# Optimization experiments

Hardware: AMD Instinct MI355X
Metric: run time of the kernel (lower is better)

The kernel has to match this reference:

```python
import jax, jax.numpy as jnp
import numpy as np

NUM_HEADS = 16

def setup_inputs() -> dict:
    key = jax.random.key(0)
    k1, k2, k3 = jax.random.split(key, 3)
    B, N, C = 4, 1024, 1024
    x = jax.random.normal(k1, (B, N, C), dtype=jnp.float32)
    w_qkv = jax.random.normal(k2, (C, 3 * C), dtype=jnp.float32) * (C ** -0.5)
    b_qkv = jnp.zeros((3 * C,), dtype=jnp.float32)
    w_proj = jax.random.normal(k3, (C, C), dtype=jnp.float32) * (C ** -0.5)
    b_proj = jnp.zeros((C,), dtype=jnp.float32)
    return {"x": x, "w_qkv": w_qkv, "b_qkv": b_qkv, "w_proj": w_proj, "b_proj": b_proj}

def reference(x, w_qkv, b_qkv, w_proj, b_proj):
    B, N, C = x.shape
    H = NUM_HEADS
    D = C // H
    scale = D ** -0.5
    # qkv projection: [B,N,3C] -> [3,B,H,N,D]
    qkv = (x @ w_qkv + b_qkv).reshape(B, N, 3, H, D).transpose(2, 0, 3, 1, 4)
    q, k, v = qkv[0], qkv[1], qkv[2]
    q = q * scale
    attn = jnp.einsum('bhnd,bhmd->bhnm', q, k)  # full N x N scores
    attn = jax.nn.softmax(attn, axis=-1)
    out = jnp.einsum('bhnm,bhmd->bhnd', attn, v)  # [B,H,N,D]
    out = out.transpose(0, 2, 1, 3).reshape(B, N, C)
    return out @ w_proj + b_proj
```

## Files before the change

kernel.cpp:

```cpp
#include <hip/hip_runtime.h>

typedef unsigned short u16;
typedef unsigned int u32;
typedef __attribute__((ext_vector_type(8))) short bf16x8;
typedef __attribute__((ext_vector_type(4))) float f32x4;
typedef __attribute__((ext_vector_type(16))) float f32x16;

#define LOG2E 1.4426950408889634f
#define QSCALE (0.125f * LOG2E)

__device__ __forceinline__ u16 f2bf(float f) {
  union { float f; u32 u; } x; x.f = f;
  u32 r = x.u + 0x7fffu + ((x.u >> 16) & 1u);
  return (u16)(r >> 16);
}

__device__ __forceinline__ u32 cvtpk(float a, float b) {
  u32 r;
  asm("v_cvt_pk_bf16_f32 %0, %1, %2" : "=v"(r) : "v"(a), "v"(b));
  return r;
}

__device__ __forceinline__ bf16x8 mkfrag(u32 a, u32 b, u32 c, u32 d) {
  union { u32 w[4]; bf16x8 v; } u;
  u.w[0] = a; u.w[1] = b; u.w[2] = c; u.w[3] = d;
  return u.v;
}

__device__ __forceinline__ void gload_lds16(const void* g, void* l) {
  __builtin_amdgcn_global_load_lds((const __attribute__((address_space(1))) u32*)g,
                                   (__attribute__((address_space(3))) u32*)l, 16, 0, 0);
}

__global__ __launch_bounds__(256) void k_cvt_x(const float* __restrict__ in, u16* __restrict__ out) {
  int i = blockIdx.x * 256 + threadIdx.x;
  const float4* p = (const float4*)in;
  float4 a = p[i * 2], b = p[i * 2 + 1];
  uint4 o;
  o.x = (u32)f2bf(a.x) | ((u32)f2bf(a.y) << 16);
  o.y = (u32)f2bf(a.z) | ((u32)f2bf(a.w) << 16);
  o.z = (u32)f2bf(b.x) | ((u32)f2bf(b.y) << 16);
  o.w = (u32)f2bf(b.z) | ((u32)f2bf(b.w) << 16);
  ((uint4*)out)[i] = o;
}

__global__ __launch_bounds__(256) void k_transpose_cvt(const float* __restrict__ src, u16* __restrict__ dst,
                                                       int R, int Cc) {
  __shared__ float tile[32][33];
  int c0 = blockIdx.x * 32, r0 = blockIdx.y * 32;
  int tx = threadIdx.x, ty = threadIdx.y;
  #pragma unroll
  for (int j = 0; j < 4; ++j)
    tile[ty * 4 + j][tx] = src[(r0 + ty * 4 + j) * Cc + c0 + tx];
  __syncthreads();
  #pragma unroll
  for (int j = 0; j < 4; ++j) {
    int cl = ty * 4 + j;
    dst[(c0 + cl) * R + r0 + tx] = f2bf(tile[tx][cl]);
  }
}

template <int EPI, int NBN>
__global__ __launch_bounds__(512) void k_gemm(const u16* __restrict__ A, const u16* __restrict__ Bt,
                                              const float* __restrict__ bias,
                                              u16* __restrict__ oq, u16* __restrict__ ok,
                                              u16* __restrict__ ovt, float* __restrict__ of) {
  __shared__ u16 lds[24576];
  const int tid = threadIdx.x;
  const int l = tid & 63, w = tid >> 6;
  const int wm = w >> 2, wn = w & 3;
  const int lr = l & 15, lh = l >> 4;
  const int cpx = gridDim.x >> 3;
  const int wg = (blockIdx.x & 7) * cpx + (blockIdx.x >> 3);
  const int bn = wg % NBN, bm = wg / NBN;

  f32x4 acc[4][2] = {};
  const int e = tid * 8;
  const int srow = e >> 5;
  const int sgr  = (e >> 3) & 3;
  const int scol = (sgr ^ ((srow >> 1) & 3)) * 8;
  const u16* gA = A + (bm * 128 + srow) * 1024 + scol;
  const u16* gB = Bt + (bn * 128 + srow) * 1024 + scol;

  #define GSTAGE(kk, b)                                              \
    do {                                                             \
      gload_lds16(gA + (kk), lds + (b) * 8192 + e);                  \
      gload_lds16(gB + (kk), lds + (b) * 8192 + 4096 + e);           \
    } while (0)

  GSTAGE(0, 0);
  GSTAGE(32, 1);
  int cur = 0, nxt = 2;

  for (int it = 0; it < 32; ++it) {
    if (it < 31) asm volatile("s_waitcnt vmcnt(2)" ::: "memory");
    else         asm volatile("s_waitcnt vmcnt(0)" ::: "memory");
    __builtin_amdgcn_s_barrier();
    __builtin_amdgcn_sched_barrier(0);

    if (it < 30) GSTAGE((it + 2) * 32, nxt);

    const u16* Asc = lds + cur * 8192;
    bf16x8 af[4], bfr[2];
    #pragma unroll
    for (int mi = 0; mi < 4; ++mi) {
      int r = wm * 64 + mi * 16 + lr;
      af[mi] = *(const bf16x8*)(Asc + r * 32 + ((lh ^ ((r >> 1) & 3)) * 8));
    }
    #pragma unroll
    for (int ni = 0; ni < 2; ++ni) {
      int r = wn * 32 + ni * 16 + lr;
      bfr[ni] = *(const bf16x8*)(Asc + 4096 + r * 32 + ((lh ^ ((r >> 1) & 3)) * 8));
    }
    #pragma unroll
    for (int mi = 0; mi < 4; ++mi)
      #pragma unroll
      for (int ni = 0; ni < 2; ++ni)
        acc[mi][ni] = __builtin_amdgcn_mfma_f32_16x16x32_bf16(af[mi], bfr[ni], acc[mi][ni], 0, 0, 0);

    cur = (cur == 2) ? 0 : cur + 1;
    nxt = (nxt == 2) ? 0 : nxt + 1;
  }
  #undef GSTAGE

  if (EPI == 0) {
    #pragma unroll
    for (int ni = 0; ni < 2; ++ni) {
      int col = bn * 128 + wn * 32 + ni * 16 + lr;
      float bb = bias[col];
      #pragma unroll
      for (int mi = 0; mi < 4; ++mi) {
        int row = bm * 128 + wm * 64 + mi * 16 + lh * 4;
        #pragma unroll
        for (int r = 0; r < 4; ++r)
          of[(row + r) * (NBN * 128) + col] = acc[mi][ni][r] + bb;
      }
    }
  } else {
    const int s = bn >> 3;
    __syncthreads();
    if (s < 2) {
      u16* dst = (s == 0) ? oq : ok;
      const float sc = (s == 0) ? QSCALE : 1.0f;
      #pragma unroll
      for (int ni = 0; ni < 2; ++ni) {
        int cl = wn * 32 + ni * 16 + lr;
        float bb = bias[bn * 128 + cl];
        #pragma unroll
        for (int mi = 0; mi < 4; ++mi) {
          int rl = wm * 64 + mi * 16 + lh * 4;
          #pragma unroll
          for (int r = 0; r < 4; ++r)
            lds[(rl + r) * 136 + cl] = f2bf((acc[mi][ni][r] + bb) * sc);
        }
      }
      __syncthreads();
      const int row = tid >> 2, q4 = tid & 3;
      const int h0 = ((bn * 128) & 1023) >> 6;
      const int b = (bm * 128) >> 10, n0 = (bm * 128) & 1023;
      const u16* srow2 = lds + row * 136 + q4 * 32;
      u16* drow = dst + ((u32)((b * 16 + h0 + (q4 >> 1)) * 1024) + n0 + row) * 64 + (q4 & 1) * 32;
      #pragma unroll
      for (int j = 0; j < 4; ++j)
        *(uint4*)(drow + j * 8) = *(const uint4*)(srow2 + j * 8);
    } else {
      #pragma unroll
      for (int ni = 0; ni < 2; ++ni) {
        int cl = wn * 32 + ni * 16 + lr;
        float bb = bias[bn * 128 + cl];
        #pragma unroll
        for (int mi = 0; mi < 4; ++mi) {
          int rl = wm * 64 + mi * 16 + lh * 4;
          u32 p0 = (u32)f2bf(acc[mi][ni][0] + bb) | ((u32)f2bf(acc[mi][ni][1] + bb) << 16);
          u32 p1 = (u32)f2bf(acc[mi][ni][2] + bb) | ((u32)f2bf(acc[mi][ni][3] + bb) << 16);
          uint2 pk; pk.x = p0; pk.y = p1;
          *(uint2*)(lds + cl * 136 + rl) = pk;
        }
      }
      __syncthreads();
      const int cl = tid >> 2, q4 = tid & 3;
      const int c = bn * 128 + cl, cc = c & 1023, h = cc >> 6, d = cc & 63;
      const int b = (bm * 128) >> 10, n0 = (bm * 128) & 1023;
      const u16* srow2 = lds + cl * 136 + q4 * 32;
      u16* drow = ovt + ((b * 16 + h) * 64 + d) * 1024 + n0 + q4 * 32;
      #pragma unroll
      for (int j = 0; j < 4; ++j)
        *(uint4*)(drow + j * 8) = *(const uint4*)(srow2 + j * 8);
    }
  }
}

__global__ __launch_bounds__(256) void k_attn(const u16* __restrict__ q, const u16* __restrict__ k,
                                              const u16* __restrict__ vt, u16* __restrict__ ao) {
  __shared__ u16 Ks[2][4096], Vs[2][4096];
  const int tid = threadIdx.x, l = tid & 63, w = tid >> 6;
  const int lq = l & 31;
  const int hi = l >> 5;
  const int i = blockIdx.x;
  const int bh = (i & 7) * 8 + ((i >> 3) & 7);
  const int qb = i >> 6;

  const int qrow = qb * 128 + w * 32 + lq;
  const u16* qg = q + bh * 65536 + qrow * 64;
  bf16x8 qf[4];
  #pragma unroll
  for (int ks = 0; ks < 4; ++ks)
    qf[ks] = *(const bf16x8*)(qg + ks * 16 + hi * 8);

  float mr = -1e30f, lsum = 0.f;
  f32x16 o0 = {}, o1 = {};

  const u16* kg = k + bh * 65536;
  const u16* vg = vt + bh * 65536;

  const int ch0 = tid, ch1 = 256 + tid;
  const int r0_ = ch0 >> 3, s0_ = (ch0 & 7) ^ (r0_ & 7);
  const int r1_ = ch1 >> 3, s1_ = (ch1 & 7) ^ (r1_ & 7);

  #define STAGE(t, buf)                                                        \
    do {                                                                       \
      gload_lds16(kg + (t) * 4096 + r0_ * 64 + s0_ * 8, Ks[buf] + ch0 * 8);    \
      gload_lds16(vg + r0_ * 1024 + (t) * 64 + s0_ * 8, Vs[buf] + ch0 * 8);    \
      gload_lds16(kg + (t) * 4096 + r1_ * 64 + s1_ * 8, Ks[buf] + ch1 * 8);    \
      gload_lds16(vg + r1_ * 1024 + (t) * 64 + s1_ * 8, Vs[buf] + ch1 * 8);    \
    } while (0)

  STAGE(0, 0);

  const int swz = (lq & 7) << 4;

  for (int t = 0; t < 16; ++t) {
    const int cur = t & 1;
    if (t < 15) {
      STAGE(t + 1, cur ^ 1);
      asm volatile("s_waitcnt vmcnt(4)" ::: "memory");
    } else {
      asm volatile("s_waitcnt vmcnt(0)" ::: "memory");
    }
    __builtin_amdgcn_s_barrier();
    __builtin_amdgcn_sched_barrier(0);

    f32x16 sA = {}, sB = {};
    __builtin_amdgcn_s_setprio(1);
    #pragma unroll
    for (int ks = 0; ks < 4; ++ks) {
      bf16x8 kf0 = *(const bf16x8*)((const char*)Ks[cur] + (((lq) * 128 + ks * 32 + hi * 16) ^ swz));
      bf16x8 kf1 = *(const bf16x8*)((const char*)Ks[cur] + (((32 + lq) * 128 + ks * 32 + hi * 16) ^ swz));
      sA = __builtin_amdgcn_mfma_f32_32x32x16_bf16(kf0, qf[ks], sA, 0, 0, 0);
      sB = __builtin_amdgcn_mfma_f32_32x32x16_bf16(kf1, qf[ks], sB, 0, 0, 0);
    }
    __builtin_amdgcn_s_setprio(0);

    float pmax = sA[0];
    #pragma unroll
    for (int r = 1; r < 16; ++r) pmax = fmaxf(pmax, sA[r]);
    #pragma unroll
    for (int r = 0; r < 16; ++r) pmax = fmaxf(pmax, sB[r]);
    pmax = fmaxf(pmax, __shfl_xor(pmax, 32));

    if (!__all(pmax - mr <= 8.0f)) {
      float nm = fmaxf(mr, pmax);
      float al = __builtin_amdgcn_exp2f(mr - nm);
      mr = nm;
      lsum *= al;
      #pragma unroll
      for (int r = 0; r < 16; ++r) {
        int row = (r & 3) + 8 * (r >> 2) + 4 * hi;
        float f = __shfl(al, row, 64);
        o0[r] *= f; o1[r] *= f;
      }
    }

    float ls = 0.f;
    #pragma unroll
    for (int r = 0; r < 16; ++r) { float e = __builtin_amdgcn_exp2f(sA[r] - mr); sA[r] = e; ls += e; }
    #pragma unroll
    for (int r = 0; r < 16; ++r) { float e = __builtin_amdgcn_exp2f(sB[r] - mr); sB[r] = e; ls += e; }
    lsum += ls;

    u32 wa[8], wb[8];
    #pragma unroll
    for (int j = 0; j < 8; ++j) {
      wa[j] = cvtpk(sA[2 * j], sA[2 * j + 1]);
      wb[j] = cvtpk(sB[2 * j], sB[2 * j + 1]);
    }
    u32 xa0 = __shfl_xor((int)wa[0], 32), xa1 = __shfl_xor((int)wa[1], 32);
    u32 xa2 = __shfl_xor((int)wa[2], 32), xa3 = __shfl_xor((int)wa[3], 32);
    u32 xa4 = __shfl_xor((int)wa[4], 32), xa5 = __shfl_xor((int)wa[5], 32);
    u32 xa6 = __shfl_xor((int)wa[6], 32), xa7 = __shfl_xor((int)wa[7], 32);
    u32 xb0 = __shfl_xor((int)wb[0], 32), xb1 = __shfl_xor((int)wb[1], 32);
    u32 xb2 = __shfl_xor((int)wb[2], 32), xb3 = __shfl_xor((int)wb[3], 32);
    u32 xb4 = __shfl_xor((int)wb[4], 32), xb5 = __shfl_xor((int)wb[5], 32);
    u32 xb6 = __shfl_xor((int)wb[6], 32), xb7 = __shfl_xor((int)wb[7], 32);
    bf16x8 pa0 = mkfrag(hi ? xa2 : wa[0], hi ? xa3 : wa[1], hi ? wa[2] : xa0, hi ? wa[3] : xa1);
    bf16x8 pa1 = mkfrag(hi ? xa6 : wa[4], hi ? xa7 : wa[5], hi ? wa[6] : xa4, hi ? wa[7] : xa5);
    bf16x8 pa2 = mkfrag(hi ? xb2 : wb[0], hi ? xb3 : wb[1], hi ? wb[2] : xb0, hi ? wb[3] : xb1);
    bf16x8 pa3 = mkfrag(hi ? xb6 : wb[4], hi ? xb7 : wb[5], hi ? wb[6] : xb4, hi ? wb[7] : xb5);

    __builtin_amdgcn_s_setprio(1);
    #pragma unroll
    for (int ks = 0; ks < 4; ++ks) {
      bf16x8 pf = (ks == 0) ? pa0 : (ks == 1) ? pa1 : (ks == 2) ? pa2 : pa3;
      bf16x8 vf0 = *(const bf16x8*)((const char*)Vs[cur] + (((lq) * 128 + ks * 32 + hi * 16) ^ swz));
      bf16x8 vf1 = *(const bf16x8*)((const char*)Vs[cur] + (((32 + lq) * 128 + ks * 32 + hi * 16) ^ swz));
      o0 = __builtin_amdgcn_mfma_f32_32x32x16_bf16(pf, vf0, o0, 0, 0, 0);
      o1 = __builtin_amdgcn_mfma_f32_32x32x16_bf16(pf, vf1, o1, 0, 0, 0);
    }
    __builtin_amdgcn_s_setprio(0);

    __builtin_amdgcn_s_barrier();
  }
  #undef STAGE

  lsum += __shfl_xor(lsum, 32);
  const int b = bh >> 4, h = bh & 15;
  u16* aob = ao + (u32)(b * 1024 + qb * 128 + w * 32) * 1024 + h * 64;
  #pragma unroll
  for (int r = 0; r < 16; ++r) {
    int row = (r & 3) + 8 * (r >> 2) + 4 * hi;
    float inv = 1.0f / __shfl(lsum, row, 64);
    aob[row * 1024 + lq]      = f2bf(o0[r] * inv);
    aob[row * 1024 + 32 + lq] = f2bf(o1[r] * inv);
  }
}

extern "C" void kernel_launch(void* const* d_in, const int* in_sizes, int n_in,
                              void* d_out, int out_size, void* d_ws, size_t ws_size,
                              hipStream_t stream) {
  const float* x      = (const float*)d_in[0];
  const float* w_qkv  = (const float*)d_in[1];
  const float* b_qkv  = (const float*)d_in[2];
  const float* w_proj = (const float*)d_in[3];
  const float* b_proj = (const float*)d_in[4];
  float* out = (float*)d_out;
  char* ws = (char*)d_ws;

  u16* X16   = (u16*)ws;
  u16* Wqkv  = (u16*)(ws + 8388608);
  u16* Wproj = (u16*)(ws + 14680064);
  u16* Q     = (u16*)(ws + 16777216);
  u16* K     = (u16*)(ws + 25165824);
  u16* VT    = (u16*)(ws + 33554432);
  u16* AO    = X16;

  k_cvt_x<<<dim3(2048), dim3(256), 0, stream>>>(x, X16);
  k_transpose_cvt<<<dim3(96, 32), dim3(32, 8), 0, stream>>>(w_qkv, Wqkv, 1024, 3072);
  k_transpose_cvt<<<dim3(32, 32), dim3(32, 8), 0, stream>>>(w_proj, Wproj, 1024, 1024);
  k_gemm<1, 24><<<dim3(768), dim3(512), 0, stream>>>(X16, Wqkv, b_qkv, Q, K, VT, (float*)0);
  k_attn<<<dim3(512), dim3(256), 0, stream>>>(Q, K, VT, AO);
  k_gemm<0, 8><<<dim3(256), dim3(512), 0, stream>>>(AO, Wproj, b_proj, (u16*)0, (u16*)0, (u16*)0, out);
}
```

Baseline: 99.87 us.

## Double the attention KV tile to 128 keys per iteration

```diff
diff --git a/kernel.cpp b/kernel.cpp
--- a/kernel.cpp
+++ b/kernel.cpp
@@ -30,6 +30,19 @@
 __device__ __forceinline__ void gload_lds16(const void* g, void* l) {
   __builtin_amdgcn_global_load_lds((const __attribute__((address_space(1))) u32*)g,
                                    (__attribute__((address_space(3))) u32*)l, 16, 0, 0);
+}
+
+__device__ __forceinline__ void packP(const f32x16& s, int hi, bf16x8& P0, bf16x8& P1) {
+  u32 w0 = cvtpk(s[0], s[1]),  w1 = cvtpk(s[2], s[3]);
+  u32 w2 = cvtpk(s[4], s[5]),  w3 = cvtpk(s[6], s[7]);
+  u32 w4 = cvtpk(s[8], s[9]),  w5 = cvtpk(s[10], s[11]);
+  u32 w6 = cvtpk(s[12], s[13]), w7 = cvtpk(s[14], s[15]);
+  u32 x0 = __shfl_xor((int)w0, 32), x1 = __shfl_xor((int)w1, 32);
+  u32 x2 = __shfl_xor((int)w2, 32), x3 = __shfl_xor((int)w3, 32);
+  u32 x4 = __shfl_xor((int)w4, 32), x5 = __shfl_xor((int)w5, 32);
+  u32 x6 = __shfl_xor((int)w6, 32), x7 = __shfl_xor((int)w7, 32);
+  P0 = mkfrag(hi ? x2 : w0, hi ? x3 : w1, hi ? w2 : x0, hi ? w3 : x1);
+  P1 = mkfrag(hi ? x6 : w4, hi ? x7 : w5, hi ? w6 : x4, hi ? w7 : x5);
 }
 
 __global__ __launch_bounds__(256) void k_cvt_x(const float* __restrict__ in, u16* __restrict__ out) {
@@ -192,7 +205,7 @@
 
 __global__ __launch_bounds__(256) void k_attn(const u16* __restrict__ q, const u16* __restrict__ k,
                                               const u16* __restrict__ vt, u16* __restrict__ ao) {
-  __shared__ u16 Ks[2][4096], Vs[2][4096];
+  __shared__ u16 Ks[2][8192], Vs[2][8192];
   const int tid = threadIdx.x, l = tid & 63, w = tid >> 6;
   const int lq = l & 31;
   const int hi = l >> 5;
@@ -213,49 +226,60 @@
   const u16* kg = k + bh * 65536;
   const u16* vg = vt + bh * 65536;
 
-  const int ch0 = tid, ch1 = 256 + tid;
-  const int r0_ = ch0 >> 3, s0_ = (ch0 & 7) ^ (r0_ & 7);
-  const int r1_ = ch1 >> 3, s1_ = (ch1 & 7) ^ (r1_ & 7);
-
-  #define STAGE(t, buf)                                                        \
-    do {                                                                       \
-      gload_lds16(kg + (t) * 4096 + r0_ * 64 + s0_ * 8, Ks[buf] + ch0 * 8);    \
-      gload_lds16(vg + r0_ * 1024 + (t) * 64 + s0_ * 8, Vs[buf] + ch0 * 8);    \
-      gload_lds16(kg + (t) * 4096 + r1_ * 64 + s1_ * 8, Ks[buf] + ch1 * 8);    \
-      gload_lds16(vg + r1_ * 1024 + (t) * 64 + s1_ * 8, Vs[buf] + ch1 * 8);    \
+  #define STAGE(t, buf)                                                             \
+    do {                                                                            \
+      _Pragma("unroll")                                                             \
+      for (int j = 0; j < 4; ++j) {                                                 \
+        int c = j * 256 + tid;                                                      \
+        int kr = c >> 3, kg_ = (c & 7) ^ (kr & 7);                                  \
+        gload_lds16(kg + (t) * 8192 + kr * 64 + kg_ * 8, Ks[buf] + c * 8);          \
+        int vr = c >> 4, vg_ = (c & 15) ^ (vr & 15);                                \
+        gload_lds16(vg + vr * 1024 + (t) * 128 + vg_ * 8, Vs[buf] + c * 8);         \
+      }                                                                             \
     } while (0)
 
   STAGE(0, 0);
 
-  const int swz = (lq & 7) << 4;
-
-  for (int t = 0; t < 16; ++t) {
+  const int kswz = (lq & 7) << 4;
+  const int vswz = (lq & 15) << 4;
+
+  for (int t = 0; t < 8; ++t) {
     const int cur = t & 1;
-    if (t < 15) {
+    if (t < 7) {
       STAGE(t + 1, cur ^ 1);
-      asm volatile("s_waitcnt vmcnt(4)" ::: "memory");
+      asm volatile("s_waitcnt vmcnt(8)" ::: "memory");
     } else {
       asm volatile("s_waitcnt vmcnt(0)" ::: "memory");
     }
     __builtin_amdgcn_s_barrier();
     __builtin_amdgcn_sched_barrier(0);
 
-    f32x16 sA = {}, sB = {};
+    f32x16 sA = {}, sB = {}, sC = {}, sD = {};
+    const char* Kb = (const char*)Ks[cur];
     __builtin_amdgcn_s_setprio(1);
     #pragma unroll
     for (int ks = 0; ks < 4; ++ks) {
-      bf16x8 kf0 = *(const bf16x8*)((const char*)Ks[cur] + (((lq) * 128 + ks * 32 + hi * 16) ^ swz));
-      bf16x8 kf1 = *(const bf16x8*)((const char*)Ks[cur] + (((32 + lq) * 128 + ks * 32 + hi * 16) ^ swz));
+      int co = ks * 32 + hi * 16;
+      bf16x8 kf0 = *(const bf16x8*)(Kb + (((lq) * 128 + co) ^ kswz));
+      bf16x8 kf1 = *(const bf16x8*)(Kb + (((32 + lq) * 128 + co) ^ kswz));
+      bf16x8 kf2 = *(const bf16x8*)(Kb + (((64 + lq) * 128 + co) ^ kswz));
+      bf16x8 kf3 = *(const bf16x8*)(Kb + (((96 + lq) * 128 + co) ^ kswz));
       sA = __builtin_amdgcn_mfma_f32_32x32x16_bf16(kf0, qf[ks], sA, 0, 0, 0);
       sB = __builtin_amdgcn_mfma_f32_32x32x16_bf16(kf1, qf[ks], sB, 0, 0, 0);
+      sC = __builtin_amdgcn_mfma_f32_32x32x16_bf16(kf2, qf[ks], sC, 0, 0, 0);
+      sD = __builtin_amdgcn_mfma_f32_32x32x16_bf16(kf3, qf[ks], sD, 0, 0, 0);
     }
     __builtin_amdgcn_s_setprio(0);
 
-    float pmax = sA[0];
-    #pragma unroll
-    for (int r = 1; r < 16; ++r) pmax = fmaxf(pmax, sA[r]);
-    #pragma unroll
-    for (int r = 0; r < 16; ++r) pmax = fmaxf(pmax, sB[r]);
+    float tm[16];
+    #pragma unroll
+    for (int r = 0; r < 16; ++r)
+      tm[r] = fmaxf(fmaxf(sA[r], sB[r]), fmaxf(sC[r], sD[r]));
+    #pragma unroll
+    for (int r = 0; r < 8; ++r) tm[r] = fmaxf(tm[r], tm[r + 8]);
+    #pragma unroll
+    for (int r = 0; r < 4; ++r) tm[r] = fmaxf(tm[r], tm[r + 4]);
+    float pmax = fmaxf(fmaxf(tm[0], tm[1]), fmaxf(tm[2], tm[3]));
     pmax = fmaxf(pmax, __shfl_xor(pmax, 32));
 
     if (!__all(pmax - mr <= 8.0f)) {
@@ -271,41 +295,35 @@
       }
     }
 
-    float ls = 0.f;
-    #pragma unroll
-    for (int r = 0; r < 16; ++r) { float e = __builtin_amdgcn_exp2f(sA[r] - mr); sA[r] = e; ls += e; }
-    #pragma unroll
-    for (int r = 0; r < 16; ++r) { float e = __builtin_amdgcn_exp2f(sB[r] - mr); sB[r] = e; ls += e; }
-    lsum += ls;
-
-    u32 wa[8], wb[8];
-    #pragma unroll
-    for (int j = 0; j < 8; ++j) {
-      wa[j] = cvtpk(sA[2 * j], sA[2 * j + 1]);
-      wb[j] = cvtpk(sB[2 * j], sB[2 * j + 1]);
-    }
-    u32 xa0 = __shfl_xor((int)wa[0], 32), xa1 = __shfl_xor((int)wa[1], 32);
-    u32 xa2 = __shfl_xor((int)wa[2], 32), xa3 = __shfl_xor((int)wa[3], 32);
-    u32 xa4 = __shfl_xor((int)wa[4], 32), xa5 = __shfl_xor((int)wa[5], 32);
-    u32 xa6 = __shfl_xor((int)wa[6], 32), xa7 = __shfl_xor((int)wa[7], 32);
-    u32 xb0 = __shfl_xor((int)wb[0], 32), xb1 = __shfl_xor((int)wb[1], 32);
-    u32 xb2 = __shfl_xor((int)wb[2], 32), xb3 = __shfl_xor((int)wb[3], 32);
-    u32 xb4 = __shfl_xor((int)wb[4], 32), xb5 = __shfl_xor((int)wb[5], 32);
-    u32 xb6 = __shfl_xor((int)wb[6], 32), xb7 = __shfl_xor((int)wb[7], 32);
-    bf16x8 pa0 = mkfrag(hi ? xa2 : wa[0], hi ? xa3 : wa[1], hi ? wa[2] : xa0, hi ? wa[3] : xa1);
-    bf16x8 pa1 = mkfrag(hi ? xa6 : wa[4], hi ? xa7 : wa[5], hi ? wa[6] : xa4, hi ? wa[7] : xa5);
-    bf16x8 pa2 = mkfrag(hi ? xb2 : wb[0], hi ? xb3 : wb[1], hi ? wb[2] : xb0, hi ? wb[3] : xb1);
-    bf16x8 pa3 = mkfrag(hi ? xb6 : wb[4], hi ? xb7 : wb[5], hi ? wb[6] : xb4, hi ? wb[7] : xb5);
-
+    float l0 = 0.f, l1 = 0.f, l2 = 0.f, l3 = 0.f;
+    #pragma unroll
+    for (int r = 0; r < 16; ++r) { float e = __builtin_amdgcn_exp2f(sA[r] - mr); sA[r] = e; l0 += e; }
+    #pragma unroll
+    for (int r = 0; r < 16; ++r) { float e = __builtin_amdgcn_exp2f(sB[r] - mr); sB[r] = e; l1 += e; }
+    #pragma unroll
+    for (int r = 0; r < 16; ++r) { float e = __builtin_amdgcn_exp2f(sC[r] - mr); sC[r] = e; l2 += e; }
+    #pragma unroll
+    for (int r = 0; r < 16; ++r) { float e = __builtin_amdgcn_exp2f(sD[r] - mr); sD[r] = e; l3 += e; }
+    lsum += (l0 + l1) + (l2 + l3);
+
+    bf16x8 pa0, pa1, pa2, pa3, pa4, pa5, pa6, pa7;
+    packP(sA, hi, pa0, pa1);
+    packP(sB, hi, pa2, pa3);
+    packP(sC, hi, pa4, pa5);
+    packP(sD, hi, pa6, pa7);
+
+    const char* Vb = (const char*)Vs[cur];
     __builtin_amdgcn_s_setprio(1);
-    #pragma unroll
-    for (int ks = 0; ks < 4; ++ks) {
-      bf16x8 pf = (ks == 0) ? pa0 : (ks == 1) ? pa1 : (ks == 2) ? pa2 : pa3;
-      bf16x8 vf0 = *(const bf16x8*)((const char*)Vs[cur] + (((lq) * 128 + ks * 32 + hi * 16) ^ swz));
-      bf16x8 vf1 = *(const bf16x8*)((const char*)Vs[cur] + (((32 + lq) * 128 + ks * 32 + hi * 16) ^ swz));
-      o0 = __builtin_amdgcn_mfma_f32_32x32x16_bf16(pf, vf0, o0, 0, 0, 0);
-      o1 = __builtin_amdgcn_mfma_f32_32x32x16_bf16(pf, vf1, o1, 0, 0, 0);
-    }
+    #define PVSTEP(g, PF)                                                            \
+      do {                                                                           \
+        bf16x8 vf0 = *(const bf16x8*)(Vb + (((lq) * 256 + (g) * 32 + hi * 16) ^ vswz));        \
+        bf16x8 vf1 = *(const bf16x8*)(Vb + (((32 + lq) * 256 + (g) * 32 + hi * 16) ^ vswz));   \
+        o0 = __builtin_amdgcn_mfma_f32_32x32x16_bf16(PF, vf0, o0, 0, 0, 0);          \
+        o1 = __builtin_amdgcn_mfma_f32_32x32x16_bf16(PF, vf1, o1, 0, 0, 0);          \
+      } while (0)
+    PVSTEP(0, pa0); PVSTEP(1, pa1); PVSTEP(2, pa2); PVSTEP(3, pa3);
+    PVSTEP(4, pa4); PVSTEP(5, pa5); PVSTEP(6, pa6); PVSTEP(7, pa7);
+    #undef PVSTEP
     __builtin_amdgcn_s_setprio(0);
 
     __builtin_amdgcn_s_barrier();
```

After: 112.6 us. 12.8% more time.

## Software-pipeline attention loop: overlap PV of tile t with QK of tile t+1

Applied to the files above, without the earlier changes.

```diff
diff --git a/kernel.cpp b/kernel.cpp
--- a/kernel.cpp
+++ b/kernel.cpp
@@ -30,6 +30,19 @@
 __device__ __forceinline__ void gload_lds16(const void* g, void* l) {
   __builtin_amdgcn_global_load_lds((const __attribute__((address_space(1))) u32*)g,
                                    (__attribute__((address_space(3))) u32*)l, 16, 0, 0);
+}
+
+__device__ __forceinline__ void packP(const f32x16& s, int hi, bf16x8& P0, bf16x8& P1) {
+  u32 w0 = cvtpk(s[0], s[1]),  w1 = cvtpk(s[2], s[3]);
+  u32 w2 = cvtpk(s[4], s[5]),  w3 = cvtpk(s[6], s[7]);
+  u32 w4 = cvtpk(s[8], s[9]),  w5 = cvtpk(s[10], s[11]);
+  u32 w6 = cvtpk(s[12], s[13]), w7 = cvtpk(s[14], s[15]);
+  u32 x0 = __shfl_xor((int)w0, 32), x1 = __shfl_xor((int)w1, 32);
+  u32 x2 = __shfl_xor((int)w2, 32), x3 = __shfl_xor((int)w3, 32);
+  u32 x4 = __shfl_xor((int)w4, 32), x5 = __shfl_xor((int)w5, 32);
+  u32 x6 = __shfl_xor((int)w6, 32), x7 = __shfl_xor((int)w7, 32);
+  P0 = mkfrag(hi ? x2 : w0, hi ? x3 : w1, hi ? w2 : x0, hi ? w3 : x1);
+  P1 = mkfrag(hi ? x6 : w4, hi ? x7 : w5, hi ? w6 : x4, hi ? w7 : x5);
 }
 
 __global__ __launch_bounds__(256) void k_cvt_x(const float* __restrict__ in, u16* __restrict__ out) {
@@ -192,7 +205,7 @@
 
 __global__ __launch_bounds__(256) void k_attn(const u16* __restrict__ q, const u16* __restrict__ k,
                                               const u16* __restrict__ vt, u16* __restrict__ ao) {
-  __shared__ u16 Ks[2][4096], Vs[2][4096];
+  __shared__ u16 Ks[2][4096], Vs[3][4096];
   const int tid = threadIdx.x, l = tid & 63, w = tid >> 6;
   const int lq = l & 31;
   const int hi = l >> 5;
@@ -209,6 +222,7 @@
 
   float mr = -1e30f, lsum = 0.f;
   f32x16 o0 = {}, o1 = {};
+  bf16x8 pa[4];
 
   const u16* kg = k + bh * 65536;
   const u16* vg = vt + bh * 65536;
@@ -217,100 +231,97 @@
   const int r0_ = ch0 >> 3, s0_ = (ch0 & 7) ^ (r0_ & 7);
   const int r1_ = ch1 >> 3, s1_ = (ch1 & 7) ^ (r1_ & 7);
 
-  #define STAGE(t, buf)                                                        \
+  #define STAGE(t, kb, vb)                                                     \
     do {                                                                       \
-      gload_lds16(kg + (t) * 4096 + r0_ * 64 + s0_ * 8, Ks[buf] + ch0 * 8);    \
-      gload_lds16(vg + r0_ * 1024 + (t) * 64 + s0_ * 8, Vs[buf] + ch0 * 8);    \
-      gload_lds16(kg + (t) * 4096 + r1_ * 64 + s1_ * 8, Ks[buf] + ch1 * 8);    \
-      gload_lds16(vg + r1_ * 1024 + (t) * 64 + s1_ * 8, Vs[buf] + ch1 * 8);    \
-    } while (0)
-
-  STAGE(0, 0);
+      gload_lds16(kg + (t) * 4096 + r0_ * 64 + s0_ * 8, Ks[kb] + ch0 * 8);     \
+      gload_lds16(kg + (t) * 4096 + r1_ * 64 + s1_ * 8, Ks[kb] + ch1 * 8);     \
+      gload_lds16(vg + r0_ * 1024 + (t) * 64 + s0_ * 8, Vs[vb] + ch0 * 8);     \
+      gload_lds16(vg + r1_ * 1024 + (t) * 64 + s1_ * 8, Vs[vb] + ch1 * 8);     \
+    } while (0)
 
   const int swz = (lq & 7) << 4;
 
-  for (int t = 0; t < 16; ++t) {
-    const int cur = t & 1;
-    if (t < 15) {
-      STAGE(t + 1, cur ^ 1);
-      asm volatile("s_waitcnt vmcnt(4)" ::: "memory");
-    } else {
-      asm volatile("s_waitcnt vmcnt(0)" ::: "memory");
-    }
+  #define QKM(kb, SA, SB)                                                      \
+    do {                                                                       \
+      const char* Kb = (const char*)Ks[kb];                                    \
+      _Pragma("unroll")                                                        \
+      for (int ks2 = 0; ks2 < 4; ++ks2) {                                      \
+        bf16x8 kf0 = *(const bf16x8*)(Kb + (((lq) * 128 + ks2 * 32 + hi * 16) ^ swz));      \
+        bf16x8 kf1 = *(const bf16x8*)(Kb + (((32 + lq) * 128 + ks2 * 32 + hi * 16) ^ swz)); \
+        SA = __builtin_amdgcn_mfma_f32_32x32x16_bf16(kf0, qf[ks2], SA, 0, 0, 0); \
+        SB = __builtin_amdgcn_mfma_f32_32x32x16_bf16(kf1, qf[ks2], SB, 0, 0, 0); \
+      }                                                                        \
+    } while (0)
+
+  #define SM(SA, SB)                                                           \
+    do {                                                                       \
+      float pmax = SA[0];                                                      \
+      _Pragma("unroll") for (int r = 1; r < 16; ++r) pmax = fmaxf(pmax, SA[r]); \
+      _Pragma("unroll") for (int r = 0; r < 16; ++r) pmax = fmaxf(pmax, SB[r]); \
+      pmax = fmaxf(pmax, __shfl_xor(pmax, 32));                                \
+      if (!__all(pmax - mr <= 8.0f)) {           \
+        float nm = fmaxf(mr, pmax);                                            \
+        float al = __builtin_amdgcn_exp2f(mr - nm);                            \
+        mr = nm; lsum *= al;                                                   \
+        _Pragma("unroll") for (int r = 0; r < 16; ++r) {                       \
+          int row = (r & 3) + 8 * (r >> 2) + 4 * hi;                           \
+          float f = __shfl(al, row, 64);                                       \
+          o0[r] *= f; o1[r] *= f;                                              \
+        }                                                                      \
+      }                                                                        \
+      float ls = 0.f;                                                          \
+      _Pragma("unroll") for (int r = 0; r < 16; ++r) { float e = __builtin_amdgcn_exp2f(SA[r] - mr); SA[r] = e; ls += e; } \
+      _Pragma("unroll") for (int r = 0; r < 16; ++r) { float e = __builtin_amdgcn_exp2f(SB[r] - mr); SB[r] = e; ls += e; } \
+      lsum += ls;                                                              \
+      packP(SA, hi, pa[0], pa[1]);                                             \
+      packP(SB, hi, pa[2], pa[3]);                                             \
+    } while (0)
+
+  #define PVM(vb)                                                              \
+    do {                                                                       \
+      const char* Vb = (const char*)Vs[vb];                                    \
+      _Pragma("unroll")                                                        \
+      for (int ks2 = 0; ks2 < 4; ++ks2) {                                      \
+        bf16x8 vf0 = *(const bf16x8*)(Vb + (((lq) * 128 + ks2 * 32 + hi * 16) ^ swz));      \
+        bf16x8 vf1 = *(const bf16x8*)(Vb + (((32 + lq) * 128 + ks2 * 32 + hi * 16) ^ swz)); \
+        o0 = __builtin_amdgcn_mfma_f32_32x32x16_bf16(pa[ks2], vf0, o0, 0, 0, 0); \
+        o1 = __builtin_amdgcn_mfma_f32_32x32x16_bf16(pa[ks2], vf1, o1, 0, 0, 0); \
+      }                                                                        \
+    } while (0)
+
+  STAGE(0, 0, 0);
+  STAGE(1, 1, 1);
+
+  asm volatile("s_waitcnt vmcnt(6)" ::: "memory");
+  __builtin_amdgcn_s_barrier();
+  __builtin_amdgcn_sched_barrier(0);
+  {
+    f32x16 sA = {}, sB = {};
+    QKM(0, sA, sB);
+    SM(sA, sB);
+  }
+
+  for (int t = 0; t < 15; ++t) {
+    const int vb = t % 3;
+    const int kb1 = (t + 1) & 1;
+    if (t < 14) asm volatile("s_waitcnt vmcnt(2)" ::: "memory");
+    else        asm volatile("s_waitcnt vmcnt(0)" ::: "memory");
     __builtin_amdgcn_s_barrier();
     __builtin_amdgcn_sched_barrier(0);
+    if (t < 14) STAGE(t + 2, (t + 2) & 1, (t + 2) % 3);
 
     f32x16 sA = {}, sB = {};
     __builtin_amdgcn_s_setprio(1);
-    #pragma unroll
-    for (int ks = 0; ks < 4; ++ks) {
-      bf16x8 kf0 = *(const bf16x8*)((const char*)Ks[cur] + (((lq) * 128 + ks * 32 + hi * 16) ^ swz));
-      bf16x8 kf1 = *(const bf16x8*)((const char*)Ks[cur] + (((32 + lq) * 128 + ks * 32 + hi * 16) ^ swz));
-      sA = __builtin_amdgcn_mfma_f32_32x32x16_bf16(kf0, qf[ks], sA, 0, 0, 0);
-      sB = __builtin_amdgcn_mfma_f32_32x32x16_bf16(kf1, qf[ks], sB, 0, 0, 0);
-    }
+    PVM(vb);
+    QKM(kb1, sA, sB);
     __builtin_amdgcn_s_setprio(0);
-
-    float pmax = sA[0];
-    #pragma unroll
-    for (int r = 1; r < 16; ++r) pmax = fmaxf(pmax, sA[r]);
-    #pragma unroll
-    for (int r = 0; r < 16; ++r) pmax = fmaxf(pmax, sB[r]);
-    pmax = fmaxf(pmax, __shfl_xor(pmax, 32));
-
-    if (!__all(pmax - mr <= 8.0f)) {
-      float nm = fmaxf(mr, pmax);
-      float al = __builtin_amdgcn_exp2f(mr - nm);
-      mr = nm;
-      lsum *= al;
-      #pragma unroll
-      for (int r = 0; r < 16; ++r) {
-        int row = (r & 3) + 8 * (r >> 2) + 4 * hi;
-        float f = __shfl(al, row, 64);
-        o0[r] *= f; o1[r] *= f;
-      }
-    }
-
-    float ls = 0.f;
-    #pragma unroll
-    for (int r = 0; r < 16; ++r) { float e = __builtin_amdgcn_exp2f(sA[r] - mr); sA[r] = e; ls += e; }
-    #pragma unroll
-    for (int r = 0; r < 16; ++r) { float e = __builtin_amdgcn_exp2f(sB[r] - mr); sB[r] = e; ls += e; }
-    lsum += ls;
-
-    u32 wa[8], wb[8];
-    #pragma unroll
-    for (int j = 0; j < 8; ++j) {
-      wa[j] = cvtpk(sA[2 * j], sA[2 * j + 1]);
-      wb[j] = cvtpk(sB[2 * j], sB[2 * j + 1]);
-    }
-    u32 xa0 = __shfl_xor((int)wa[0], 32), xa1 = __shfl_xor((int)wa[1], 32);
-    u32 xa2 = __shfl_xor((int)wa[2], 32), xa3 = __shfl_xor((int)wa[3], 32);
-    u32 xa4 = __shfl_xor((int)wa[4], 32), xa5 = __shfl_xor((int)wa[5], 32);
-    u32 xa6 = __shfl_xor((int)wa[6], 32), xa7 = __shfl_xor((int)wa[7], 32);
-    u32 xb0 = __shfl_xor((int)wb[0], 32), xb1 = __shfl_xor((int)wb[1], 32);
-    u32 xb2 = __shfl_xor((int)wb[2], 32), xb3 = __shfl_xor((int)wb[3], 32);
-    u32 xb4 = __shfl_xor((int)wb[4], 32), xb5 = __shfl_xor((int)wb[5], 32);
-    u32 xb6 = __shfl_xor((int)wb[6], 32), xb7 = __shfl_xor((int)wb[7], 32);
-    bf16x8 pa0 = mkfrag(hi ? xa2 : wa[0], hi ? xa3 : wa[1], hi ? wa[2] : xa0, hi ? wa[3] : xa1);
-    bf16x8 pa1 = mkfrag(hi ? xa6 : wa[4], hi ? xa7 : wa[5], hi ? wa[6] : xa4, hi ? wa[7] : xa5);
-    bf16x8 pa2 = mkfrag(hi ? xb2 : wb[0], hi ? xb3 : wb[1], hi ? wb[2] : xb0, hi ? wb[3] : xb1);
-    bf16x8 pa3 = mkfrag(hi ? xb6 : wb[4], hi ? xb7 : wb[5], hi ? wb[6] : xb4, hi ? wb[7] : xb5);
-
-    __builtin_amdgcn_s_setprio(1);
-    #pragma unroll
-    for (int ks = 0; ks < 4; ++ks) {
-      bf16x8 pf = (ks == 0) ? pa0 : (ks == 1) ? pa1 : (ks == 2) ? pa2 : pa3;
-      bf16x8 vf0 = *(const bf16x8*)((const char*)Vs[cur] + (((lq) * 128 + ks * 32 + hi * 16) ^ swz));
-      bf16x8 vf1 = *(const bf16x8*)((const char*)Vs[cur] + (((32 + lq) * 128 + ks * 32 + hi * 16) ^ swz));
-      o0 = __builtin_amdgcn_mfma_f32_32x32x16_bf16(pf, vf0, o0, 0, 0, 0);
-      o1 = __builtin_amdgcn_mfma_f32_32x32x16_bf16(pf, vf1, o1, 0, 0, 0);
-    }
-    __builtin_amdgcn_s_setprio(0);
-
-    __builtin_amdgcn_s_barrier();
-  }
+    SM(sA, sB);
+  }
+  PVM(0);
   #undef STAGE
+  #undef QKM
+  #undef SM
+  #undef PVM
 
   lsum += __shfl_xor(lsum, 32);
   const int b = bh >> 4, h = bh & 15;
```

After: 100.0 us. No clear change (+0.2%).
